# Kernel tuning notes

Hardware: AMD Instinct MI355X
Metric: run time of the kernel (lower is better)

Reference implementation:

```python
import jax, jax.numpy as jnp
import numpy as np

VOCAB_SIZE = 4096
D_EMBED = 256
BETA = 0.25  # unused: module returns raw commit_loss; beta applied by caller


def setup_inputs() -> dict:
    key = jax.random.key(0)
    k_h, k_e = jax.random.split(key)
    h = jax.random.normal(k_h, (16, D_EMBED, 32, 32), dtype=jnp.float32)
    embedding = jax.random.normal(k_e, (VOCAB_SIZE, D_EMBED), dtype=jnp.float32)
    return {"h": h, "embedding": embedding}


def reference(h, embedding):
    B, C, H, W = h.shape
    h = h.astype(jnp.float32)
    # (B, C, H, W) -> (N, C) with N = B*H*W
    h_flat = jnp.transpose(h, (0, 2, 3, 1)).reshape(-1, C)
    dist = (
        jnp.sum(h_flat * h_flat, axis=1, keepdims=True)
        + jnp.sum(embedding * embedding, axis=1)
        - 2.0 * jnp.einsum("nc,vc->nv", h_flat, embedding)
    )
    indices_flat = jnp.argmin(dist, axis=1)
    indices = indices_flat.reshape(B, H, W)
    # gather codebook vectors and restore (B, C, H, W)
    z_q = jnp.transpose(embedding[indices_flat].reshape(B, H, W, C), (0, 3, 1, 2))
    commit_loss = jnp.mean((h - jax.lax.stop_gradient(z_q)) ** 2)
    # straight-through estimator
    z_q_st = h + jax.lax.stop_gradient(z_q - h)
    return z_q_st, indices, commit_loss
```

## Files before the change

kernel.cpp:

```cpp
#include <hip/hip_runtime.h>

#define D 256
#define VOCAB 4096
#define NTOT 16384
#define N_OUT0 4194304

typedef _Float16 half8 __attribute__((ext_vector_type(8)));
typedef float f32x4 __attribute__((ext_vector_type(4)));

__device__ __forceinline__ void gld16(const void* g, void* l) {
    __builtin_amdgcn_global_load_lds(
        (const __attribute__((address_space(1))) void*)g,
        (__attribute__((address_space(3))) void*)l, 16, 0, 0);
}

__device__ __forceinline__ unsigned long long pack_key(float d, int v) {
    unsigned u = __float_as_uint(d);
    u ^= ((unsigned)((int)u >> 31)) | 0x80000000u;
    return ((unsigned long long)u << 32) | (unsigned)v;
}

__global__ __launch_bounds__(256) void k_pack(const float* __restrict__ h,
                                              const float* __restrict__ emb,
                                              _Float16* __restrict__ Apk,
                                              _Float16* __restrict__ Bpk,
                                              float* __restrict__ esq,
                                              unsigned long long* __restrict__ gbest,
                                              float* __restrict__ out2) {
    __shared__ float S[8192];
    const int tid = threadIdx.x;
    const int bid = blockIdx.x;
    if (bid < 512) {
        const int bm = bid >> 3, w = bid & 7;
        const int b = bm >> 2, p0 = (bm & 3) * 256;
        const float* src = h + ((size_t)b << 18) + p0;
#pragma unroll 4
        for (int cl = 0; cl < 32; ++cl)
            S[cl * 256 + tid] = src[(size_t)(w * 32 + cl) << 10 | (unsigned)tid];
        __syncthreads();
        _Float16* dstT = Apk + (size_t)bm * 131072 + (size_t)w * 16384;
#pragma unroll
        for (int i = 0; i < 4; ++i) {
            alignas(16) _Float16 hi[8], lo[8];
#pragma unroll
            for (int j = 0; j < 8; ++j) {
                float vv = S[(i * 8 + j) * 256 + tid];
                _Float16 hv = (_Float16)vv;
                hi[j] = hv;
                lo[j] = (_Float16)(vv - (float)hv);
            }
            _Float16* dst = dstT + i * 2048 + tid * 8;
            *(half8*)dst = *(half8*)hi;
            *(half8*)(dst + 8192) = *(half8*)lo;
        }
    } else if (bid < 768) {
        const int bid2 = bid - 512;
        const int bn = bid2 >> 3, w = bid2 & 7;
        const int v0 = bn * 128;
#pragma unroll 4
        for (int i = 0; i < 16; ++i) {
            int flat = i * 256 + tid;
            int r = flat >> 5, cl = flat & 31;
            S[cl * 129 + r] = emb[(size_t)(v0 + r) * D + w * 32 + cl];
        }
        __syncthreads();
        _Float16* dstT = Bpk + (size_t)bn * 65536 + (size_t)w * 8192;
#pragma unroll
        for (int i = 0; i < 2; ++i) {
            int s = i * 256 + tid;
            int q = s >> 7, r = s & 127;
            alignas(16) _Float16 hi[8], lo[8];
#pragma unroll
            for (int j = 0; j < 8; ++j) {
                float vv = S[(q * 8 + j) * 129 + r];
                _Float16 hv = (_Float16)vv;
                hi[j] = hv;
                lo[j] = (_Float16)(vv - (float)hv);
            }
            _Float16* dst = dstT + q * 1024 + r * 8;
            *(half8*)dst = *(half8*)hi;
            *(half8*)(dst + 4096) = *(half8*)lo;
        }
    } else {
        const int pid = bid - 768;
        const int lane = tid & 63, wv = tid >> 6;
#pragma unroll 4
        for (int i = 0; i < 16; ++i) {
            int v = pid * 64 + i * 4 + wv;
            float4 e = *(const float4*)(emb + (size_t)v * D + lane * 4);
            float s = e.x * e.x + e.y * e.y + e.z * e.z + e.w * e.w;
#pragma unroll
            for (int m = 32; m >= 1; m >>= 1) s += __shfl_xor(s, m, 64);
            if (lane == 0) esq[v] = s;
        }
        gbest[pid * 256 + tid] = ~0ULL;
        if (pid == 0 && tid == 0) out2[0] = 0.0f;
    }
}


#define STAGE_A(W) do { _Pragma("unroll") \
    for (int it_ = 0; it_ < 4; ++it_) { \
        int f_ = it_ * 256 + tid; \
        gld16(AgH + (W) * 16384 + (f_ >> 9) * 8192 + ((f_ >> 7) & 3) * 2048 + (f_ & 127) * 8, \
              As + f_ * 8); \
    } } while (0)
#define STAGE_B(W, NB) do { _Pragma("unroll") \
    for (int it_ = 0; it_ < 4; ++it_) { \
        int f_ = it_ * 256 + tid; \
        gld16(Bg + (W) * 8192 + f_ * 8, Bs + (NB) + f_ * 8); \
    } } while (0)

#define LOAD_AF(OFF) do { _Pragma("unroll") \
    for (int mt_ = 0; mt_ < 4; ++mt_) af[mt_] = *(const half8*)(aB + (OFF) + mt_ * 128); } while (0)
#define LOAD_BF(OFF) do { _Pragma("unroll") \
    for (int nt_ = 0; nt_ < 4; ++nt_) bf[nt_] = *(const half8*)(bB + (OFF) + nt_ * 128); } while (0)

#define MFMA16() do { \
    __builtin_amdgcn_s_setprio(1); \
    _Pragma("unroll") \
    for (int mt_ = 0; mt_ < 4; ++mt_) { \
      _Pragma("unroll") \
      for (int nt_ = 0; nt_ < 4; ++nt_) \
        acc[mt_][nt_] = __builtin_amdgcn_mfma_f32_16x16x32_f16(af[mt_], bf[nt_], acc[mt_][nt_], 0, 0, 0); \
    } \
    __builtin_amdgcn_s_setprio(0); \
  } while (0)

__global__ __launch_bounds__(256, 3) void k_gemm(const _Float16* __restrict__ Apk,
                                                 const _Float16* __restrict__ Bpk,
                                                 const float* __restrict__ esq,
                                                 unsigned long long* __restrict__ gbest) {
    __shared__ alignas(16) _Float16 As[8192];
    __shared__ alignas(16) _Float16 Bs[16384];

    const int tid = threadIdx.x;
    const int bid = blockIdx.x;
    const int swz = (bid & 7) * 512 + (bid >> 3);
    const int bm = swz >> 5, bn = swz & 31;
    const int m0 = bm * 128, n0 = bn * 128;

    const _Float16* AgH = Apk + (size_t)(bm >> 1) * 131072 + (size_t)(bm & 1) * 1024;
    const _Float16* Bg = Bpk + (size_t)bn * 65536;

    STAGE_A(0);
    STAGE_B(0, 0);

    const int wv = tid >> 6, l = tid & 63;
    const int wm = wv & 1, wn = wv >> 1;
    const int quad = l >> 4, j16 = l & 15;
    const _Float16* aB = As + quad * 1024 + (wm * 64 + j16) * 8;

    f32x4 acc[4][4];
#pragma unroll
    for (int i = 0; i < 4; ++i)
#pragma unroll
        for (int j = 0; j < 4; ++j) acc[i][j] = (f32x4)0.0f;

    __syncthreads();

#pragma unroll 1
    for (int w = 0; w < 8; ++w) {
        const int cb = (w & 1) << 13, nb = cb ^ 8192;
        const _Float16* bB = Bs + cb + quad * 1024 + (wn * 64 + j16) * 8;
        if (w < 7) STAGE_B(w + 1, nb);
        half8 af[4], bf[4];
        LOAD_AF(0);
        LOAD_BF(4096);
        MFMA16();
        LOAD_BF(0);
        MFMA16();
        LOAD_AF(4096);
        if (w < 7) {
            __syncthreads();
            STAGE_A(w + 1);
        }
        MFMA16();
        __syncthreads();
    }

    unsigned long long* red = (unsigned long long*)As;
    if (tid < 128) red[tid] = ~0ULL;
    __syncthreads();

    float es[4];
    int vidx[4];
#pragma unroll
    for (int nt = 0; nt < 4; ++nt) {
        vidx[nt] = n0 + wn * 64 + nt * 16 + j16;
        es[nt] = esq[vidx[nt]];
    }
#pragma unroll
    for (int mt = 0; mt < 4; ++mt) {
#pragma unroll
        for (int r = 0; r < 4; ++r) {
            unsigned long long best = ~0ULL;
#pragma unroll
            for (int nt = 0; nt < 4; ++nt) {
                float dv = es[nt] - 2.0f * acc[mt][nt][r];
                unsigned long long key = pack_key(dv, vidx[nt]);
                best = key < best ? key : best;
            }
#pragma unroll
            for (int m = 8; m >= 1; m >>= 1) {
                unsigned long long o = __shfl_xor(best, m, 64);
                best = o < best ? o : best;
            }
            if (j16 == 0) atomicMin(&red[wm * 64 + mt * 16 + quad * 4 + r], best);
        }
    }
    __syncthreads();
    if (tid < 128) atomicMin(&gbest[m0 + tid], red[tid]);
}

__global__ __launch_bounds__(256) void k_gather(const float* __restrict__ h,
                                                const float* __restrict__ emb,
                                                const unsigned long long* __restrict__ gbest,
                                                float* __restrict__ out0,
                                                float* __restrict__ out1,
                                                float* __restrict__ out2) {
    __shared__ float zq[32][260];
    __shared__ float wred[4];
    const int tid = threadIdx.x;
    const int lane = tid & 63;
    const int w = tid >> 6;
    const int n0 = blockIdx.x * 32;
    const int b = n0 >> 10;
    const int p0 = n0 & 1023;
#pragma unroll
    for (int rr = 0; rr < 8; ++rr) {
        int r = w * 8 + rr;
        unsigned idx = (unsigned)(gbest[n0 + r] & 0xFFFFFFFFULL);
        float4 e4 = *(const float4*)(emb + (size_t)idx * D + lane * 4);
        *(float4*)&zq[r][lane * 4] = e4;
    }
    if (tid < 32) {
        unsigned idx = (unsigned)(gbest[n0 + tid] & 0xFFFFFFFFULL);
        out1[n0 + tid] = (float)idx;
    }
    __syncthreads();
    float lsum = 0.0f;
    const size_t base = ((size_t)b * D) << 10;
#pragma unroll 4
    for (int it = 0; it < 32; ++it) {
        int c = it * 8 + (tid >> 5);
        int pp = tid & 31;
        float z = zq[pp][c];
        size_t g = base + ((size_t)c << 10) + p0 + pp;
        float hv = h[g];
        out0[g] = hv + (z - hv);
        float d = hv - z;
        lsum = fmaf(d, d, lsum);
    }
#pragma unroll
    for (int m = 32; m >= 1; m >>= 1) lsum += __shfl_xor(lsum, m, 64);
    if (lane == 0) wred[w] = lsum;
    __syncthreads();
    if (tid == 0)
        atomicAdd(out2, (wred[0] + wred[1] + wred[2] + wred[3]) * (1.0f / (float)N_OUT0));
}

extern "C" void kernel_launch(void* const* d_in, const int* in_sizes, int n_in,
                              void* d_out, int out_size, void* d_ws, size_t ws_size,
                              hipStream_t stream) {
    const float* h = (const float*)d_in[0];
    const float* emb = (const float*)d_in[1];
    float* out0 = (float*)d_out;
    float* out1 = out0 + N_OUT0;
    float* out2 = out1 + NTOT;

    _Float16* Apk = (_Float16*)d_ws;
    _Float16* Bpk = (_Float16*)((char*)d_ws + 16777216);
    float* esq = (float*)((char*)d_ws + 16777216 + 4194304);
    unsigned long long* gbest = (unsigned long long*)((char*)d_ws + 16777216 + 4194304 + 16384);

    hipLaunchKernelGGL(k_pack, dim3(832), dim3(256), 0, stream, h, emb, Apk, Bpk, esq, gbest, out2);
    hipLaunchKernelGGL(k_gemm, dim3(4096), dim3(256), 0, stream, Apk, Bpk, esq, gbest);
    hipLaunchKernelGGL(k_gather, dim3(NTOT / 32), dim3(256), 0, stream, h, emb, gbest, out0, out1, out2);
}
```

Baseline: 202.7 us.

## Replace split-fp16 GEMM with single fp16 pass plus exact top-2 rescoring

New measurement: 306.5 us. +51.2%, slower.

```diff
diff --git a/kernel.cpp b/kernel.cpp
--- a/kernel.cpp
+++ b/kernel.cpp
@@ -7,6 +7,7 @@
 
 typedef _Float16 half8 __attribute__((ext_vector_type(8)));
 typedef float f32x4 __attribute__((ext_vector_type(4)));
+typedef unsigned long long u64;
 
 __device__ __forceinline__ void gld16(const void* g, void* l) {
     __builtin_amdgcn_global_load_lds(
@@ -14,19 +15,51 @@
         (__attribute__((address_space(3))) void*)l, 16, 0, 0);
 }
 
-__device__ __forceinline__ unsigned long long pack_key(float d, int v) {
+__device__ __forceinline__ u64 pack_key(float d, int v) {
     unsigned u = __float_as_uint(d);
     u ^= ((unsigned)((int)u >> 31)) | 0x80000000u;
-    return ((unsigned long long)u << 32) | (unsigned)v;
+    return ((u64)u << 32) | (unsigned)v;
+}
+
+__device__ __forceinline__ float unpack_dist(u64 k) {
+    unsigned u = (unsigned)(k >> 32);
+    u = (u & 0x80000000u) ? (u ^ 0x80000000u) : ~u;
+    return __uint_as_float(u);
+}
+
+__global__ __launch_bounds__(256) void k_prep(const float* __restrict__ emb,
+                                              float* __restrict__ esq,
+                                              float* __restrict__ e2maxp,
+                                              float* __restrict__ out2) {
+    __shared__ float sm[4];
+    const int tid = threadIdx.x, lane = tid & 63, wv = tid >> 6;
+    const int v0 = blockIdx.x * 64;
+    float lmax = 0.0f;
+#pragma unroll 4
+    for (int i = 0; i < 16; ++i) {
+        int v = v0 + i * 4 + wv;
+        float4 e = *(const float4*)(emb + (size_t)v * D + lane * 4);
+        float s = e.x * e.x + e.y * e.y + e.z * e.z + e.w * e.w;
+#pragma unroll
+        for (int m = 32; m >= 1; m >>= 1) s += __shfl_xor(s, m, 64);
+        if (lane == 0) esq[v] = s;
+        lmax = fmaxf(lmax, s);
+    }
+    if (lane == 0) sm[wv] = lmax;
+    __syncthreads();
+    if (tid == 0) {
+        e2maxp[blockIdx.x] = fmaxf(fmaxf(sm[0], sm[1]), fmaxf(sm[2], sm[3]));
+        if (blockIdx.x == 0) out2[0] = 0.0f;
+    }
 }
 
 __global__ __launch_bounds__(256) void k_pack(const float* __restrict__ h,
                                               const float* __restrict__ emb,
                                               _Float16* __restrict__ Apk,
                                               _Float16* __restrict__ Bpk,
-                                              float* __restrict__ esq,
-                                              unsigned long long* __restrict__ gbest,
-                                              float* __restrict__ out2) {
+                                              float* __restrict__ hsqp,
+                                              const float* __restrict__ e2maxp,
+                                              float* __restrict__ E2max) {
     __shared__ float S[8192];
     const int tid = threadIdx.x;
     const int bid = blockIdx.x;
@@ -38,20 +71,20 @@
         for (int cl = 0; cl < 32; ++cl)
             S[cl * 256 + tid] = src[(size_t)(w * 32 + cl) << 10 | (unsigned)tid];
         __syncthreads();
-        _Float16* dstT = Apk + (size_t)bm * 131072 + (size_t)w * 16384;
+        float sq = 0.0f;
+#pragma unroll
+        for (int cl = 0; cl < 32; ++cl) {
+            float t = S[cl * 256 + tid];
+            sq = fmaf(t, t, sq);
+        }
+        hsqp[(size_t)(bm * 8 + w) * 256 + tid] = sq;
+        _Float16* dstT = Apk + (size_t)bm * 65536 + (size_t)w * 8192;
 #pragma unroll
         for (int i = 0; i < 4; ++i) {
-            alignas(16) _Float16 hi[8], lo[8];
-#pragma unroll
-            for (int j = 0; j < 8; ++j) {
-                float vv = S[(i * 8 + j) * 256 + tid];
-                _Float16 hv = (_Float16)vv;
-                hi[j] = hv;
-                lo[j] = (_Float16)(vv - (float)hv);
-            }
-            _Float16* dst = dstT + i * 2048 + tid * 8;
-            *(half8*)dst = *(half8*)hi;
-            *(half8*)(dst + 8192) = *(half8*)lo;
+            alignas(16) _Float16 hi[8];
+#pragma unroll
+            for (int j = 0; j < 8; ++j) hi[j] = (_Float16)S[(i * 8 + j) * 256 + tid];
+            *(half8*)(dstT + i * 2048 + tid * 8) = *(half8*)hi;
         }
     } else if (bid < 768) {
         const int bid2 = bid - 512;
@@ -64,59 +97,54 @@
             S[cl * 129 + r] = emb[(size_t)(v0 + r) * D + w * 32 + cl];
         }
         __syncthreads();
-        _Float16* dstT = Bpk + (size_t)bn * 65536 + (size_t)w * 8192;
+        _Float16* dstT = Bpk + (size_t)bn * 32768 + (size_t)w * 4096;
 #pragma unroll
         for (int i = 0; i < 2; ++i) {
             int s = i * 256 + tid;
             int q = s >> 7, r = s & 127;
-            alignas(16) _Float16 hi[8], lo[8];
-#pragma unroll
-            for (int j = 0; j < 8; ++j) {
-                float vv = S[(q * 8 + j) * 129 + r];
-                _Float16 hv = (_Float16)vv;
-                hi[j] = hv;
-                lo[j] = (_Float16)(vv - (float)hv);
-            }
-            _Float16* dst = dstT + q * 1024 + r * 8;
-            *(half8*)dst = *(half8*)hi;
-            *(half8*)(dst + 4096) = *(half8*)lo;
+            alignas(16) _Float16 hi[8];
+#pragma unroll
+            for (int j = 0; j < 8; ++j) hi[j] = (_Float16)S[(q * 8 + j) * 129 + r];
+            *(half8*)(dstT + q * 1024 + r * 8) = *(half8*)hi;
         }
     } else {
-        const int pid = bid - 768;
-        const int lane = tid & 63, wv = tid >> 6;
-#pragma unroll 4
-        for (int i = 0; i < 16; ++i) {
-            int v = pid * 64 + i * 4 + wv;
-            float4 e = *(const float4*)(emb + (size_t)v * D + lane * 4);
-            float s = e.x * e.x + e.y * e.y + e.z * e.z + e.w * e.w;
-#pragma unroll
-            for (int m = 32; m >= 1; m >>= 1) s += __shfl_xor(s, m, 64);
-            if (lane == 0) esq[v] = s;
-        }
-        gbest[pid * 256 + tid] = ~0ULL;
-        if (pid == 0 && tid == 0) out2[0] = 0.0f;
-    }
-}
-
-
-#define STAGE_A(W) do { _Pragma("unroll") \
-    for (int it_ = 0; it_ < 4; ++it_) { \
-        int f_ = it_ * 256 + tid; \
-        gld16(AgH + (W) * 16384 + (f_ >> 9) * 8192 + ((f_ >> 7) & 3) * 2048 + (f_ & 127) * 8, \
-              As + f_ * 8); \
+        if (tid < 64) {
+            float m = e2maxp[tid];
+#pragma unroll
+            for (int s = 32; s >= 1; s >>= 1) m = fmaxf(m, __shfl_xor(m, s, 64));
+            if (tid == 0) E2max[0] = m;
+        }
+    }
+}
+
+
+#define STAGE(W, BUF) do { \
+    _Pragma("unroll") \
+    for (int s_ = 0; s_ < 2; ++s_) { \
+        int f_ = s_ * 256 + tid; \
+        gld16(AgH + (W) * 8192 + (f_ >> 7) * 2048 + (f_ & 127) * 8, \
+              As + (BUF) * 4096 + f_ * 8); \
+    } \
+    _Pragma("unroll") \
+    for (int s_ = 0; s_ < 2; ++s_) { \
+        int f_ = s_ * 256 + tid; \
+        gld16(Bg + (W) * 4096 + f_ * 8, Bs + (BUF) * 4096 + f_ * 8); \
     } } while (0)
-#define STAGE_B(W, NB) do { _Pragma("unroll") \
-    for (int it_ = 0; it_ < 4; ++it_) { \
-        int f_ = it_ * 256 + tid; \
-        gld16(Bg + (W) * 8192 + f_ * 8, Bs + (NB) + f_ * 8); \
-    } } while (0)
-
-#define LOAD_AF(OFF) do { _Pragma("unroll") \
-    for (int mt_ = 0; mt_ < 4; ++mt_) af[mt_] = *(const half8*)(aB + (OFF) + mt_ * 128); } while (0)
-#define LOAD_BF(OFF) do { _Pragma("unroll") \
-    for (int nt_ = 0; nt_ < 4; ++nt_) bf[nt_] = *(const half8*)(bB + (OFF) + nt_ * 128); } while (0)
-
-#define MFMA16() do { \
+
+#define PHASE_END(N) do { \
+    __builtin_amdgcn_sched_barrier(0); \
+    asm volatile("s_waitcnt vmcnt(" #N ")" ::: "memory"); \
+    __builtin_amdgcn_s_barrier(); } while (0)
+
+#define WINDOW(BUF, DOSTAGE, SW, SBUF) do { \
+    const _Float16* aB = As + (BUF) * 4096 + quad * 1024 + (wm * 64 + j16) * 8; \
+    const _Float16* bB = Bs + (BUF) * 4096 + quad * 1024 + (wn * 64 + j16) * 8; \
+    if (DOSTAGE) STAGE(SW, SBUF); \
+    half8 af[4], bf[4]; \
+    _Pragma("unroll") \
+    for (int mt_ = 0; mt_ < 4; ++mt_) af[mt_] = *(const half8*)(aB + mt_ * 128); \
+    _Pragma("unroll") \
+    for (int nt_ = 0; nt_ < 4; ++nt_) bf[nt_] = *(const half8*)(bB + nt_ * 128); \
     __builtin_amdgcn_s_setprio(1); \
     _Pragma("unroll") \
     for (int mt_ = 0; mt_ < 4; ++mt_) { \
@@ -130,9 +158,9 @@
 __global__ __launch_bounds__(256, 3) void k_gemm(const _Float16* __restrict__ Apk,
                                                  const _Float16* __restrict__ Bpk,
                                                  const float* __restrict__ esq,
-                                                 unsigned long long* __restrict__ gbest) {
-    __shared__ alignas(16) _Float16 As[8192];
-    __shared__ alignas(16) _Float16 Bs[16384];
+                                                 u64* __restrict__ keys2) {
+    __shared__ alignas(16) _Float16 As[12288];
+    __shared__ alignas(16) _Float16 Bs[12288];
 
     const int tid = threadIdx.x;
     const int bid = blockIdx.x;
@@ -140,16 +168,15 @@
     const int bm = swz >> 5, bn = swz & 31;
     const int m0 = bm * 128, n0 = bn * 128;
 
-    const _Float16* AgH = Apk + (size_t)(bm >> 1) * 131072 + (size_t)(bm & 1) * 1024;
-    const _Float16* Bg = Bpk + (size_t)bn * 65536;
-
-    STAGE_A(0);
-    STAGE_B(0, 0);
+    const _Float16* AgH = Apk + (size_t)(bm >> 1) * 65536 + (size_t)(bm & 1) * 1024;
+    const _Float16* Bg = Bpk + (size_t)bn * 32768;
+
+    STAGE(0, 0);
+    STAGE(1, 1);
 
     const int wv = tid >> 6, l = tid & 63;
     const int wm = wv & 1, wn = wv >> 1;
     const int quad = l >> 4, j16 = l & 15;
-    const _Float16* aB = As + quad * 1024 + (wm * 64 + j16) * 8;
 
     f32x4 acc[4][4];
 #pragma unroll
@@ -157,32 +184,20 @@
 #pragma unroll
         for (int j = 0; j < 4; ++j) acc[i][j] = (f32x4)0.0f;
 
-    __syncthreads();
-
-#pragma unroll 1
-    for (int w = 0; w < 8; ++w) {
-        const int cb = (w & 1) << 13, nb = cb ^ 8192;
-        const _Float16* bB = Bs + cb + quad * 1024 + (wn * 64 + j16) * 8;
-        if (w < 7) STAGE_B(w + 1, nb);
-        half8 af[4], bf[4];
-        LOAD_AF(0);
-        LOAD_BF(4096);
-        MFMA16();
-        LOAD_BF(0);
-        MFMA16();
-        LOAD_AF(4096);
-        if (w < 7) {
-            __syncthreads();
-            STAGE_A(w + 1);
-        }
-        MFMA16();
-        __syncthreads();
-    }
-
-    unsigned long long* red = (unsigned long long*)As;
-    if (tid < 128) red[tid] = ~0ULL;
-    __syncthreads();
-
+    asm volatile("s_waitcnt vmcnt(4)" ::: "memory");
+    __builtin_amdgcn_s_barrier();
+
+    WINDOW(0, 1, 2, 2); PHASE_END(4);
+    WINDOW(1, 1, 3, 0); PHASE_END(4);
+    WINDOW(2, 1, 4, 1); PHASE_END(4);
+    WINDOW(0, 1, 5, 2); PHASE_END(4);
+    WINDOW(1, 1, 6, 0); PHASE_END(4);
+    WINDOW(2, 1, 7, 1); PHASE_END(4);
+    WINDOW(0, 0, 0, 0); PHASE_END(0);
+    WINDOW(1, 0, 0, 0);
+    __syncthreads();
+
+    u64* t2 = (u64*)As;
     float es[4];
     int vidx[4];
 #pragma unroll
@@ -194,28 +209,64 @@
     for (int mt = 0; mt < 4; ++mt) {
 #pragma unroll
         for (int r = 0; r < 4; ++r) {
-            unsigned long long best = ~0ULL;
+            u64 m1 = ~0ULL, m2 = ~0ULL;
 #pragma unroll
             for (int nt = 0; nt < 4; ++nt) {
                 float dv = es[nt] - 2.0f * acc[mt][nt][r];
-                unsigned long long key = pack_key(dv, vidx[nt]);
-                best = key < best ? key : best;
+                u64 k = pack_key(dv, vidx[nt]);
+                if (k < m1) { m2 = m1; m1 = k; }
+                else if (k < m2) { m2 = k; }
             }
 #pragma unroll
             for (int m = 8; m >= 1; m >>= 1) {
-                unsigned long long o = __shfl_xor(best, m, 64);
-                best = o < best ? o : best;
+                u64 o1 = __shfl_xor(m1, m, 64), o2 = __shfl_xor(m2, m, 64);
+                u64 hi = m1 > o1 ? m1 : o1;
+                m1 = m1 < o1 ? m1 : o1;
+                u64 lo2 = m2 < o2 ? m2 : o2;
+                m2 = hi < lo2 ? hi : lo2;
             }
-            if (j16 == 0) atomicMin(&red[wm * 64 + mt * 16 + quad * 4 + r], best);
-        }
-    }
-    __syncthreads();
-    if (tid < 128) atomicMin(&gbest[m0 + tid], red[tid]);
+            if (j16 == 0) {
+                int row = wm * 64 + mt * 16 + quad * 4 + r;
+                t2[row * 4 + wn * 2 + 0] = m1;
+                t2[row * 4 + wn * 2 + 1] = m2;
+            }
+        }
+    }
+    __syncthreads();
+    if (tid < 128) {
+        u64 a1 = t2[tid * 4 + 0], a2 = t2[tid * 4 + 1];
+        u64 b1 = t2[tid * 4 + 2], b2 = t2[tid * 4 + 3];
+        u64 M1 = a1 < b1 ? a1 : b1;
+        u64 x = a1 < b1 ? b1 : a1;
+        u64 y = a2 < b2 ? a2 : b2;
+        u64 M2 = x < y ? x : y;
+        keys2[(size_t)bn * (NTOT * 2) + (size_t)(m0 + tid) * 2 + 0] = M1;
+        keys2[(size_t)bn * (NTOT * 2) + (size_t)(m0 + tid) * 2 + 1] = M2;
+    }
+}
+
+__device__ __forceinline__ u64 exact_key(const float* __restrict__ h,
+                                         const float* __restrict__ emb,
+                                         const float* __restrict__ esq,
+                                         int rg, int v, int lane) {
+    const float* hb = h + (((size_t)(rg >> 10)) << 18) + (rg & 1023);
+    const float4 e4 = *(const float4*)(emb + (size_t)v * D + lane * 4);
+    float p = 0.0f;
+    p = fmaf(hb[(size_t)(lane * 4 + 0) << 10], e4.x, p);
+    p = fmaf(hb[(size_t)(lane * 4 + 1) << 10], e4.y, p);
+    p = fmaf(hb[(size_t)(lane * 4 + 2) << 10], e4.z, p);
+    p = fmaf(hb[(size_t)(lane * 4 + 3) << 10], e4.w, p);
+#pragma unroll
+    for (int m = 32; m >= 1; m >>= 1) p += __shfl_xor(p, m, 64);
+    return pack_key(esq[v] - 2.0f * p, v);
 }
 
 __global__ __launch_bounds__(256) void k_gather(const float* __restrict__ h,
                                                 const float* __restrict__ emb,
-                                                const unsigned long long* __restrict__ gbest,
+                                                const float* __restrict__ esq,
+                                                const float* __restrict__ hsqp,
+                                                const float* __restrict__ E2max,
+                                                const u64* __restrict__ keys2,
                                                 float* __restrict__ out0,
                                                 float* __restrict__ out1,
                                                 float* __restrict__ out2) {
@@ -227,18 +278,46 @@
     const int n0 = blockIdx.x * 32;
     const int b = n0 >> 10;
     const int p0 = n0 & 1023;
-#pragma unroll
+    const float e2m = E2max[0];
+
+#pragma unroll 1
     for (int rr = 0; rr < 8; ++rr) {
-        int r = w * 8 + rr;
-        unsigned idx = (unsigned)(gbest[n0 + r] & 0xFFFFFFFFULL);
-        float4 e4 = *(const float4*)(emb + (size_t)idx * D + lane * 4);
-        *(float4*)&zq[r][lane * 4] = e4;
-    }
-    if (tid < 32) {
-        unsigned idx = (unsigned)(gbest[n0 + tid] & 0xFFFFFFFFULL);
-        out1[n0 + tid] = (float)idx;
-    }
-    __syncthreads();
+        const int rloc = w * 8 + rr, rg = n0 + rloc;
+        u64 key = keys2[(size_t)(lane >> 1) * (NTOT * 2) + (size_t)rg * 2 + (lane & 1)];
+        u64 gm = key;
+#pragma unroll
+        for (int m = 32; m >= 1; m >>= 1) {
+            u64 o = __shfl_xor(gm, m, 64);
+            gm = o < gm ? o : gm;
+        }
+        float hq = 0.0f;
+#pragma unroll
+        for (int k = 0; k < 8; ++k) hq += hsqp[(size_t)(rg >> 8) * 2048 + k * 256 + (rg & 255)];
+        const float thr = unpack_dist(gm) + 4.0e-3f * sqrtf(hq * e2m) + 1e-2f;
+        u64 cmask = __ballot(unpack_dist(key) <= thr);
+        u64 bestk = ~0ULL;
+        while (cmask) {
+            int L = __ffsll((long long)cmask) - 1;
+            cmask &= cmask - 1;
+            u64 kL = __shfl(key, L, 64);
+            if (L & 1) {
+                int vb = (L >> 1) * 128;
+                for (int v = vb; v < vb + 128; ++v) {
+                    u64 ek = exact_key(h, emb, esq, rg, v, lane);
+                    bestk = ek < bestk ? ek : bestk;
+                }
+            } else {
+                u64 ek = exact_key(h, emb, esq, rg, (int)(kL & 0xFFFFFFFFu), lane);
+                bestk = ek < bestk ? ek : bestk;
+            }
+        }
+        const int bidx = (int)(bestk & 0xFFFFFFFFu);
+        if (lane == 0) out1[rg] = (float)bidx;
+        float4 e4 = *(const float4*)(emb + (size_t)bidx * D + lane * 4);
+        *(float4*)&zq[rloc][lane * 4] = e4;
+    }
+    __syncthreads();
+
     float lsum = 0.0f;
     const size_t base = ((size_t)b * D) << 10;
 #pragma unroll 4
@@ -269,12 +348,17 @@
     float* out1 = out0 + N_OUT0;
     float* out2 = out1 + NTOT;
 
-    _Float16* Apk = (_Float16*)d_ws;
-    _Float16* Bpk = (_Float16*)((char*)d_ws + 16777216);
-    float* esq = (float*)((char*)d_ws + 16777216 + 4194304);
-    unsigned long long* gbest = (unsigned long long*)((char*)d_ws + 16777216 + 4194304 + 16384);
-
-    hipLaunchKernelGGL(k_pack, dim3(832), dim3(256), 0, stream, h, emb, Apk, Bpk, esq, gbest, out2);
-    hipLaunchKernelGGL(k_gemm, dim3(4096), dim3(256), 0, stream, Apk, Bpk, esq, gbest);
-    hipLaunchKernelGGL(k_gather, dim3(NTOT / 32), dim3(256), 0, stream, h, emb, gbest, out0, out1, out2);
-}
+    char* wsb = (char*)d_ws;
+    _Float16* Apk = (_Float16*)wsb;
+    _Float16* Bpk = (_Float16*)(wsb + 8388608);
+    float* esq = (float*)(wsb + 10485760);
+    float* hsqp = (float*)(wsb + 10502144);
+    float* e2maxp = (float*)(wsb + 11026432);
+    float* E2max = (float*)(wsb + 11027456);
+    u64* keys2 = (u64*)(wsb + 11028480);
+
+    hipLaunchKernelGGL(k_prep, dim3(64), dim3(256), 0, stream, emb, esq, e2maxp, out2);
+    hipLaunchKernelGGL(k_pack, dim3(769), dim3(256), 0, stream, h, emb, Apk, Bpk, hsqp, e2maxp, E2max);
+    hipLaunchKernelGGL(k_gemm, dim3(4096), dim3(256), 0, stream, Apk, Bpk, esq, keys2);
+    hipLaunchKernelGGL(k_gather, dim3(NTOT / 32), dim3(256), 0, stream, h, emb, esq, hsqp, E2max, keys2, out0, out1, out2);
+}
```
